# Kernel tuning notes

Hardware: AMD Instinct MI355X
Metric: run time of the kernel (lower is better)

The kernel has to match this reference:

```python
import jax, jax.numpy as jnp
import numpy as np

VOXEL_SIZE = np.array([0.05, 0.05, 0.1], dtype=np.float32)
PCR = np.array([0.0, -40.0, -3.0, 70.4, 40.0, 1.0], dtype=np.float32)
MAX_POINTS = 32
MAX_VOXELS = 120000
N_POINTS = 2_000_000
NFEAT = 4

GRID = np.round((PCR[3:] - PCR[:3]) / VOXEL_SIZE).astype(np.int64)  # [gx, gy, gz] = [1408, 1600, 40]
GX, GY, GZ = int(GRID[0]), int(GRID[1]), int(GRID[2])
G_TOTAL = GX * GY * GZ  # sentinel linear id for invalid points


def setup_inputs() -> dict:
    key = jax.random.key(0)
    k1, k2 = jax.random.split(key)
    # xyz uniform inside the point-cloud range, reflectivity ~ U[0,1)
    xyz = jax.random.uniform(k1, (N_POINTS, 3), minval=jnp.asarray(PCR[:3]), maxval=jnp.asarray(PCR[3:]))
    feat = jax.random.uniform(k2, (N_POINTS, NFEAT - 3))
    points = jnp.concatenate([xyz, feat], axis=1).astype(jnp.float32)
    return {"points": points}


def reference(points):
    """Deterministic hard voxelization (mmcv hard_voxelize_forward).

    Returns padded fixed-shape outputs plus voxel_num (jit-compatible):
      voxels [MAX_VOXELS, MAX_POINTS, C], coors [MAX_VOXELS, 3] (z,y,x),
      num_points_per_voxel [MAX_VOXELS], voxel_num scalar.
    Rows >= voxel_num are zero padding (torch version slices them off).
    """
    N, C = points.shape
    vs = jnp.asarray(VOXEL_SIZE)
    lo = jnp.asarray(PCR[:3])

    # Voxel coordinate of each point (x, y, z order)
    c = jnp.floor((points[:, :3] - lo) / vs).astype(jnp.int32)  # [N,3]
    valid = jnp.all((c >= 0) & (c < jnp.array([GX, GY, GZ], jnp.int32)), axis=1)

    # Linear voxel id; invalid points -> sentinel G_TOTAL (sorts last)
    lin = (c[:, 2].astype(jnp.int64) * (GY * GX)
           + c[:, 1].astype(jnp.int64) * GX
           + c[:, 0].astype(jnp.int64))
    lin = jnp.where(valid, lin, G_TOTAL)

    # Stable sort by voxel id: within a voxel, points keep original order
    order = jnp.argsort(lin, stable=True)          # [N] original indices
    slin = lin[order]
    pos = jnp.arange(N)
    is_new = jnp.concatenate([jnp.array([True]), slin[1:] != slin[:-1]])  # group starts
    start_pos = jax.lax.cummax(jnp.where(is_new, pos, 0))  # start position of each point's group
    rank_in_group = pos - start_pos                         # arrival order within voxel
    valid_s = slin < G_TOTAL

    # Voxel slots are assigned in order of first point appearance (deterministic CUDA kernel).
    # At each group start, the group's first original point index is order[pos].
    group_key = jnp.where(is_new & valid_s, order, N)       # non-starts/invalid rank last
    slot_at_pos = jnp.argsort(jnp.argsort(group_key))       # rank among groups by first appearance
    slot = slot_at_pos[start_pos]                            # [N] voxel slot per point

    voxel_num = jnp.minimum(jnp.sum((is_new & valid_s).astype(jnp.int32)), MAX_VOXELS)

    keep = valid_s & (rank_in_group < MAX_POINTS) & (slot < MAX_VOXELS)
    slot_w = jnp.where(keep, slot, MAX_VOXELS)   # dropped points -> extra pad row
    rank_w = jnp.where(keep, rank_in_group, 0)

    voxels = jnp.zeros((MAX_VOXELS + 1, MAX_POINTS, C), points.dtype)
    voxels = voxels.at[slot_w, rank_w].set(points[order])[:MAX_VOXELS]

    czyx = c[order][:, ::-1]  # store coords in (z, y, x) order like mmcv
    coor_keep = is_new & valid_s & (slot < MAX_VOXELS)
    cslot = jnp.where(coor_keep, slot, MAX_VOXELS)
    coors = jnp.zeros((MAX_VOXELS + 1, 3), jnp.int32).at[cslot].set(czyx)[:MAX_VOXELS]

    num_points_per_voxel = (jnp.zeros((MAX_VOXELS + 1,), jnp.int32)
                            .at[slot_w].add(keep.astype(jnp.int32))[:MAX_VOXELS])

    return voxels, coors, num_points_per_voxel, voxel_num
```

## Files before the change

### kernel.cpp

```cpp
#include <hip/hip_runtime.h>


#define GX 1408
#define GY 1600
#define GZ 40
#define MAXV 120000
#define MAXP 32

#define BINSHIFT 15
#define NB 2750
#define BCAP 1024
#define TSIZE 2048
#define TMASK (TSIZE - 1)
#define PB 4

#define ABLK 512
#define APT 16
#define EMIT_SPB 8

typedef unsigned long long u64;
typedef unsigned int u32;
#define EMPTY64 0xFFFFFFFFFFFFFFFFull

__device__ __forceinline__ u32 hashw(u32 lin) {
  return (lin * 2654435761u) >> 21 & TMASK;
}

__global__ __launch_bounds__(ABLK) void k_bin(const float4* __restrict__ pts,
                                              u64* __restrict__ pairs,
                                              u32* __restrict__ bincnt, int n) {
  __shared__ u32 hist[NB];
  __shared__ u32 cursor[NB];
  int tid = threadIdx.x;
  for (int b = tid; b < NB; b += ABLK) hist[b] = 0;
  __syncthreads();

  int base0 = blockIdx.x * (ABLK * APT) + tid;
  int lin[APT];
#pragma unroll
  for (int j = 0; j < APT; ++j) {
    int i = base0 + j * ABLK;
    lin[j] = -1;
    if (i < n) {
      float4 p = pts[i];
      int cx = (int)floorf((p.x - 0.0f)   / 0.05f);
      int cy = (int)floorf((p.y - -40.0f) / 0.05f);
      int cz = (int)floorf((p.z - -3.0f)  / 0.1f);
      if ((cx >= 0) && (cx < GX) && (cy >= 0) && (cy < GY) && (cz >= 0) && (cz < GZ)) {
        lin[j] = cz * (GX * GY) + cy * GX + cx;
        atomicAdd(&hist[(u32)lin[j] >> BINSHIFT], 1u);
      }
    }
  }
  __syncthreads();
  for (int b = tid; b < NB; b += ABLK) {
    u32 c = hist[b];
    cursor[b] = c ? atomicAdd(&bincnt[b], c) : 0u;
  }
  __syncthreads();
#pragma unroll
  for (int j = 0; j < APT; ++j) {
    if (lin[j] >= 0) {
      int i = base0 + j * ABLK;
      u32 b = (u32)lin[j] >> BINSHIFT;
      u32 pos = atomicAdd(&cursor[b], 1u);
      if (pos < BCAP) pairs[(size_t)b * BCAP + pos] = ((u64)(u32)lin[j] << 32) | (u32)i;
    }
  }
}

__global__ __launch_bounds__(256) void k_build(const u64* __restrict__ pairs,
                                               const u32* __restrict__ bincnt,
                                               u32* __restrict__ Lvals,
                                               unsigned char* __restrict__ isleader) {
  __shared__ u64 tab[TSIZE];
  int tid = threadIdx.x;
  int b = blockIdx.x;
  for (int s = tid; s < TSIZE; s += 256) tab[s] = EMPTY64;
  __syncthreads();

  u32 cnt = bincnt[b];
  if (cnt > BCAP) cnt = BCAP;
  size_t base = (size_t)b * BCAP;

  for (u32 c0 = 0; c0 < cnt; c0 += 256u * PB) {
    u64 pr[PB]; u32 hh[PB]; u64 old[PB];
#pragma unroll
    for (int k = 0; k < PB; ++k) {
      u32 idx = c0 + tid + (u32)k * 256u;
      pr[k] = (idx < cnt) ? pairs[base + idx] : EMPTY64;
    }
#pragma unroll
    for (int k = 0; k < PB; ++k) {
      if (pr[k] != EMPTY64) {
        hh[k] = hashw((u32)(pr[k] >> 32));
        old[k] = atomicCAS(&tab[hh[k]], EMPTY64, pr[k]);
      }
    }
#pragma unroll
    for (int k = 0; k < PB; ++k) {
      if (pr[k] != EMPTY64) {
        u32 lin = (u32)(pr[k] >> 32), i = (u32)pr[k];
        u32 s = hh[k];
        u64 o = old[k];
        while (o != EMPTY64) {
          if ((u32)(o >> 32) == lin) {
            while ((u32)o > i) {
              u64 want = (o & 0xFFFFFFFF00000000ull) | (u64)i;
              u64 prev = atomicCAS(&tab[s], o, want);
              if (prev == o) break;
              o = prev;
            }
            break;
          }
          s = (s + 1) & TMASK;
          o = atomicCAS(&tab[s], EMPTY64, pr[k]);
        }
      }
    }
  }
  __syncthreads();

  for (u32 c0 = 0; c0 < cnt; c0 += 256u * PB) {
    u64 pr[PB];
#pragma unroll
    for (int k = 0; k < PB; ++k) {
      u32 idx = c0 + tid + (u32)k * 256u;
      pr[k] = (idx < cnt) ? pairs[base + idx] : EMPTY64;
    }
#pragma unroll
    for (int k = 0; k < PB; ++k) {
      if (pr[k] != EMPTY64) {
        u32 idx = c0 + tid + (u32)k * 256u;
        u32 lin = (u32)(pr[k] >> 32), i = (u32)pr[k];
        u32 s = hashw(lin);
        u64 e = tab[s];
        while ((u32)(e >> 32) != lin) { s = (s + 1) & TMASK; e = tab[s]; }
        u32 L = (u32)e;
        Lvals[base + idx] = L;
        if (L == i) isleader[i] = 1;
      }
    }
  }
}

__global__ __launch_bounds__(256) void k_rankA(const unsigned char* __restrict__ isl,
                                               u32* __restrict__ flag,
                                               u32* __restrict__ bsum, int nwords) {
  __shared__ u32 red[256];
  int t = threadIdx.x;
  int w = blockIdx.x * 256 + t;
  u32 bits = 0;
  if (w < nwords) {
    const uint4* p = (const uint4*)(isl + (size_t)w * 32);
    uint4 a = p[0], b4 = p[1];
    u32 wd[8] = {a.x, a.y, a.z, a.w, b4.x, b4.y, b4.z, b4.w};
#pragma unroll
    for (int k = 0; k < 8; ++k) {
      u32 v = wd[k];
      bits |= (((v >> 0) & 1u) | ((v >> 8) & 1u) << 1 |
               ((v >> 16) & 1u) << 2 | ((v >> 24) & 1u) << 3) << (4 * k);
    }
    flag[w] = bits;
  }
  red[t] = __popc(bits);
  __syncthreads();
  for (int off = 128; off > 0; off >>= 1) {
    if (t < off) red[t] += red[t + off];
    __syncthreads();
  }
  if (t == 0) bsum[blockIdx.x] = red[0];
}

__global__ __launch_bounds__(256) void k_rankB(u32* __restrict__ bsum,
                                               float* __restrict__ voxnum_out,
                                               int* __restrict__ lmax, int nbk) {
  __shared__ u32 sm[256];
  int t = threadIdx.x;
  u32 v = (t < nbk) ? bsum[t] : 0;
  sm[t] = v;
  __syncthreads();
  for (int off = 1; off < 256; off <<= 1) {
    u32 x = sm[t];
    u32 add = (t >= off) ? sm[t - off] : 0;
    __syncthreads();
    sm[t] = x + add;
    __syncthreads();
  }
  if (t < nbk) bsum[t] = sm[t] - v;
  if (t == 255) {
    u32 total = sm[255];
    *voxnum_out = (float)(total < MAXV ? total : (u32)MAXV);
    if (total < MAXV) *lmax = 0x7FFFFFFF;
  }
}

__global__ __launch_bounds__(256) void k_rankC(const u32* __restrict__ flag,
                                               const u32* __restrict__ bsum,
                                               u32* __restrict__ wordpfx,
                                               int* __restrict__ lmax, int nwords) {
  __shared__ u32 sm[256];
  int t = threadIdx.x;
  int w = blockIdx.x * 256 + t;
  u32 bits = (w < nwords) ? flag[w] : 0u;
  u32 c = __popc(bits);
  sm[t] = c;
  __syncthreads();
  for (int off = 1; off < 256; off <<= 1) {
    u32 x = sm[t];
    u32 add = (t >= off) ? sm[t - off] : 0;
    __syncthreads();
    sm[t] = x + add;
    __syncthreads();
  }
  u32 p = bsum[blockIdx.x] + sm[t] - c;
  if (w < nwords) {
    wordpfx[w] = p;
    if (p < MAXV && p + c >= MAXV) {
      int kth = MAXV - 1 - (int)p;
      u32 ww = bits;
      while (kth > 0) { ww &= ww - 1; --kth; }
      *lmax = (w << 5) | (__ffs(ww) - 1);
    }
  }
}

__global__ __launch_bounds__(256) void k_keep(const u64* __restrict__ pairs,
                                              const u32* __restrict__ bincnt,
                                              const u32* __restrict__ Lvals,
                                              const u32* __restrict__ flag,
                                              const u32* __restrict__ wordpfx,
                                              const int* __restrict__ lmaxp,
                                              int* __restrict__ bcnt,
                                              int* __restrict__ bucket,
                                              float* __restrict__ out_coors) {
  int tid = threadIdx.x;
  int b = blockIdx.x;
  u32 Lmax = (u32)*lmaxp;
  u32 cnt = bincnt[b];
  if (cnt > BCAP) cnt = BCAP;
  size_t base = (size_t)b * BCAP;

  for (u32 j = tid; j < cnt; j += 256) {
    u32 L = Lvals[base + j];
    if (L > Lmax) continue;
    u64 pr = pairs[base + j];
    u32 lin = (u32)(pr >> 32), i = (u32)pr;
    u32 w = L >> 5;
    u32 r = wordpfx[w] + __popc(flag[w] & ((1u << (L & 31)) - 1u));
    int pos = atomicAdd(&bcnt[r], 1);
    if (pos < MAXP) bucket[r * MAXP + pos] = (int)i;
    if (i == L) {
      int li = (int)lin;
      int x = li % GX;
      int t2 = li / GX;
      int y = t2 % GY;
      int z = t2 / GY;
      out_coors[r * 3 + 0] = (float)z;
      out_coors[r * 3 + 1] = (float)y;
      out_coors[r * 3 + 2] = (float)x;
    }
  }
}

__global__ __launch_bounds__(256) void k_emit(const float4* __restrict__ pts,
                                              const int* __restrict__ bcnt,
                                              const int* __restrict__ bucket,
                                              float4* __restrict__ out_voxels,
                                              float* __restrict__ out_npts) {
  __shared__ int sb[EMIT_SPB][MAXP];
  int grp = threadIdx.x >> 5;
  int r = threadIdx.x & 31;
  int s = blockIdx.x * EMIT_SPB + grp;
  if (s >= MAXV) return;

  int nfull = bcnt[s];
  int m = nfull < MAXP ? nfull : MAXP;
  if (r < m) sb[grp][r] = bucket[s * MAXP + r];
  __syncthreads();

  float4 row = make_float4(0.f, 0.f, 0.f, 0.f);
  if (r < m) {
    int mine = -1;
    for (int jj = 0; jj < m; ++jj) {
      int ej = sb[grp][jj];
      int rk = 0;
      for (int kk2 = 0; kk2 < m; ++kk2) rk += (sb[grp][kk2] < ej) ? 1 : 0;
      if (rk == r) mine = ej;
    }
    row = pts[mine];
  }
  out_voxels[(size_t)s * MAXP + r] = row;
  if (r == 0) out_npts[s] = (float)m;
}

extern "C" void kernel_launch(void* const* d_in, const int* in_sizes, int n_in,
                              void* d_out, int out_size, void* d_ws, size_t ws_size,
                              hipStream_t stream) {
  const float4* pts = (const float4*)d_in[0];
  int n = in_sizes[0] / 4;
  float* out = (float*)d_out;
  int nwords = (n + 31) / 32;
  int nbk = (nwords + 255) / 256;

  char* ws = (char*)d_ws;
  size_t off = 0;
  u64* pairs    = (u64*)(ws + off); off += (size_t)NB * BCAP * 8;
  u32* Lvals    = (u32*)(ws + off); off += (size_t)NB * BCAP * 4;
  unsigned char* isleader = (unsigned char*)(ws + off); off += (size_t)n;
  u32* flag     = (u32*)(ws + off); off += 262144;
  u32* wordpfx  = (u32*)(ws + off); off += 262144;
  u32* bsum     = (u32*)(ws + off); off += 1024;
  u32* bincnt   = (u32*)(ws + off); off += 16384;
  int* lmax     = (int*)(ws + off); off += 64;
  int* bcnt     = (int*)(ws + off); off += (size_t)MAXV * 4;
  int* bucket   = (int*)(ws + off); off += (size_t)MAXV * MAXP * 4;

  float* out_voxels = out;
  float* out_coors  = out + (size_t)MAXV * MAXP * 4;
  float* out_npts   = out_coors + (size_t)MAXV * 3;

  hipMemsetAsync(bincnt, 0, 16384, stream);
  hipMemsetAsync(isleader, 0, (size_t)n, stream);
  hipMemsetAsync(bcnt, 0, (size_t)MAXV * 4, stream);
  hipMemsetAsync(out_coors, 0, ((size_t)MAXV * 3 + MAXV + 1) * sizeof(float), stream);

  int nb_bin = (n + ABLK * APT - 1) / (ABLK * APT);

  k_bin<<<nb_bin, ABLK, 0, stream>>>(pts, pairs, bincnt, n);
  k_build<<<NB, 256, 0, stream>>>(pairs, bincnt, Lvals, isleader);
  k_rankA<<<nbk, 256, 0, stream>>>(isleader, flag, bsum, nwords);
  k_rankB<<<1, 256, 0, stream>>>(bsum, out_npts + MAXV, lmax, nbk);
  k_rankC<<<nbk, 256, 0, stream>>>(flag, bsum, wordpfx, lmax, nwords);
  k_keep<<<NB, 256, 0, stream>>>(pairs, bincnt, Lvals, flag, wordpfx, lmax,
                                 bcnt, bucket, out_coors);
  k_emit<<<(MAXV + EMIT_SPB - 1) / EMIT_SPB, 256, 0, stream>>>(
      pts, bcnt, bucket, (float4*)out_voxels, out_npts);
}
```

Measured before the change: 175.8 us.

## Replace single-pass binning with two-level coarse/fine partition and fold rankB into rankC

```diff
diff --git a/kernel.cpp b/kernel.cpp
--- a/kernel.cpp
+++ b/kernel.cpp
@@ -7,15 +7,18 @@
 #define MAXV 120000
 #define MAXP 32
 
-#define BINSHIFT 15
-#define NB 2750
+#define CSHIFT 19
+#define NCB 172
+#define CCAP 14336
+#define FSHIFT 15
+#define NFB 2750
 #define BCAP 1024
 #define TSIZE 2048
 #define TMASK (TSIZE - 1)
 #define PB 4
 
 #define ABLK 512
-#define APT 16
+#define APT 8
 #define EMIT_SPB 8
 
 typedef unsigned long long u64;
@@ -26,13 +29,13 @@
   return (lin * 2654435761u) >> 21 & TMASK;
 }
 
-__global__ __launch_bounds__(ABLK) void k_bin(const float4* __restrict__ pts,
-                                              u64* __restrict__ pairs,
-                                              u32* __restrict__ bincnt, int n) {
-  __shared__ u32 hist[NB];
-  __shared__ u32 cursor[NB];
+__global__ __launch_bounds__(ABLK) void k_binA(const float4* __restrict__ pts,
+                                               u64* __restrict__ cpairs,
+                                               u32* __restrict__ ccnt, int n) {
+  __shared__ u32 hist[NCB];
+  __shared__ u32 cursor[NCB];
   int tid = threadIdx.x;
-  for (int b = tid; b < NB; b += ABLK) hist[b] = 0;
+  if (tid < NCB) hist[tid] = 0;
   __syncthreads();
 
   int base0 = blockIdx.x * (ABLK * APT) + tid;
@@ -48,29 +51,58 @@
       int cz = (int)floorf((p.z - -3.0f)  / 0.1f);
       if ((cx >= 0) && (cx < GX) && (cy >= 0) && (cy < GY) && (cz >= 0) && (cz < GZ)) {
         lin[j] = cz * (GX * GY) + cy * GX + cx;
-        atomicAdd(&hist[(u32)lin[j] >> BINSHIFT], 1u);
+        atomicAdd(&hist[(u32)lin[j] >> CSHIFT], 1u);
       }
     }
   }
   __syncthreads();
-  for (int b = tid; b < NB; b += ABLK) {
-    u32 c = hist[b];
-    cursor[b] = c ? atomicAdd(&bincnt[b], c) : 0u;
+  if (tid < NCB) {
+    u32 c = hist[tid];
+    cursor[tid] = c ? atomicAdd(&ccnt[tid], c) : 0u;
   }
   __syncthreads();
 #pragma unroll
   for (int j = 0; j < APT; ++j) {
     if (lin[j] >= 0) {
       int i = base0 + j * ABLK;
-      u32 b = (u32)lin[j] >> BINSHIFT;
-      u32 pos = atomicAdd(&cursor[b], 1u);
-      if (pos < BCAP) pairs[(size_t)b * BCAP + pos] = ((u64)(u32)lin[j] << 32) | (u32)i;
-    }
-  }
-}
-
-__global__ __launch_bounds__(256) void k_build(const u64* __restrict__ pairs,
-                                               const u32* __restrict__ bincnt,
+      u32 c = (u32)lin[j] >> CSHIFT;
+      u32 pos = atomicAdd(&cursor[c], 1u);
+      if (pos < CCAP) cpairs[(size_t)c * CCAP + pos] = ((u64)(u32)lin[j] << 32) | (u32)i;
+    }
+  }
+}
+
+__global__ __launch_bounds__(1024) void k_binB(const u64* __restrict__ cpairs,
+                                               const u32* __restrict__ ccnt,
+                                               u64* __restrict__ fpairs,
+                                               u32* __restrict__ fcnt) {
+  __shared__ u32 fh[16], fcur[16];
+  int tid = threadIdx.x;
+  int c = blockIdx.x;
+  if (tid < 16) { fh[tid] = 0; fcur[tid] = 0; }
+  __syncthreads();
+
+  u32 cnt = ccnt[c];
+  if (cnt > CCAP) cnt = CCAP;
+  size_t base = (size_t)c * CCAP;
+
+  for (u32 j = tid; j < cnt; j += 1024) {
+    u32 lin = (u32)(cpairs[base + j] >> 32);
+    atomicAdd(&fh[(lin >> FSHIFT) & 15], 1u);
+  }
+  __syncthreads();
+  if (tid < 16 && c * 16 + tid < NFB) fcnt[c * 16 + tid] = fh[tid];
+  __syncthreads();
+  for (u32 j = tid; j < cnt; j += 1024) {
+    u64 pr = cpairs[base + j];
+    u32 f = ((u32)(pr >> 32) >> FSHIFT) & 15;
+    u32 pos = atomicAdd(&fcur[f], 1u);
+    if (pos < BCAP) fpairs[(size_t)(c * 16 + f) * BCAP + pos] = pr;
+  }
+}
+
+__global__ __launch_bounds__(256) void k_build(const u64* __restrict__ fpairs,
+                                               const u32* __restrict__ fcnt,
                                                u32* __restrict__ Lvals,
                                                unsigned char* __restrict__ isleader) {
   __shared__ u64 tab[TSIZE];
@@ -79,67 +111,57 @@
   for (int s = tid; s < TSIZE; s += 256) tab[s] = EMPTY64;
   __syncthreads();
 
-  u32 cnt = bincnt[b];
+  u32 cnt = fcnt[b];
   if (cnt > BCAP) cnt = BCAP;
   size_t base = (size_t)b * BCAP;
 
-  for (u32 c0 = 0; c0 < cnt; c0 += 256u * PB) {
-    u64 pr[PB]; u32 hh[PB]; u64 old[PB];
-#pragma unroll
-    for (int k = 0; k < PB; ++k) {
-      u32 idx = c0 + tid + (u32)k * 256u;
-      pr[k] = (idx < cnt) ? pairs[base + idx] : EMPTY64;
-    }
-#pragma unroll
-    for (int k = 0; k < PB; ++k) {
-      if (pr[k] != EMPTY64) {
-        hh[k] = hashw((u32)(pr[k] >> 32));
-        old[k] = atomicCAS(&tab[hh[k]], EMPTY64, pr[k]);
+  u64 pr[PB]; u32 hh[PB]; u64 old[PB];
+#pragma unroll
+  for (int k = 0; k < PB; ++k) {
+    u32 idx = (u32)tid + (u32)k * 256u;
+    pr[k] = (idx < cnt) ? fpairs[base + idx] : EMPTY64;
+  }
+#pragma unroll
+  for (int k = 0; k < PB; ++k) {
+    if (pr[k] != EMPTY64) {
+      hh[k] = hashw((u32)(pr[k] >> 32));
+      old[k] = atomicCAS(&tab[hh[k]], EMPTY64, pr[k]);
+    }
+  }
+#pragma unroll
+  for (int k = 0; k < PB; ++k) {
+    if (pr[k] != EMPTY64) {
+      u32 lin = (u32)(pr[k] >> 32), i = (u32)pr[k];
+      u32 s = hh[k];
+      u64 o = old[k];
+      while (o != EMPTY64) {
+        if ((u32)(o >> 32) == lin) {
+          while ((u32)o > i) {
+            u64 want = (o & 0xFFFFFFFF00000000ull) | (u64)i;
+            u64 prev = atomicCAS(&tab[s], o, want);
+            if (prev == o) break;
+            o = prev;
+          }
+          break;
+        }
+        s = (s + 1) & TMASK;
+        o = atomicCAS(&tab[s], EMPTY64, pr[k]);
       }
     }
-#pragma unroll
-    for (int k = 0; k < PB; ++k) {
-      if (pr[k] != EMPTY64) {
-        u32 lin = (u32)(pr[k] >> 32), i = (u32)pr[k];
-        u32 s = hh[k];
-        u64 o = old[k];
-        while (o != EMPTY64) {
-          if ((u32)(o >> 32) == lin) {
-            while ((u32)o > i) {
-              u64 want = (o & 0xFFFFFFFF00000000ull) | (u64)i;
-              u64 prev = atomicCAS(&tab[s], o, want);
-              if (prev == o) break;
-              o = prev;
-            }
-            break;
-          }
-          s = (s + 1) & TMASK;
-          o = atomicCAS(&tab[s], EMPTY64, pr[k]);
-        }
-      }
-    }
-  }
-  __syncthreads();
-
-  for (u32 c0 = 0; c0 < cnt; c0 += 256u * PB) {
-    u64 pr[PB];
-#pragma unroll
-    for (int k = 0; k < PB; ++k) {
-      u32 idx = c0 + tid + (u32)k * 256u;
-      pr[k] = (idx < cnt) ? pairs[base + idx] : EMPTY64;
-    }
-#pragma unroll
-    for (int k = 0; k < PB; ++k) {
-      if (pr[k] != EMPTY64) {
-        u32 idx = c0 + tid + (u32)k * 256u;
-        u32 lin = (u32)(pr[k] >> 32), i = (u32)pr[k];
-        u32 s = hashw(lin);
-        u64 e = tab[s];
-        while ((u32)(e >> 32) != lin) { s = (s + 1) & TMASK; e = tab[s]; }
-        u32 L = (u32)e;
-        Lvals[base + idx] = L;
-        if (L == i) isleader[i] = 1;
-      }
+  }
+  __syncthreads();
+
+#pragma unroll
+  for (int k = 0; k < PB; ++k) {
+    if (pr[k] != EMPTY64) {
+      u32 idx = (u32)tid + (u32)k * 256u;
+      u32 lin = (u32)(pr[k] >> 32), i = (u32)pr[k];
+      u32 s = hashw(lin);
+      u64 e = tab[s];
+      while ((u32)(e >> 32) != lin) { s = (s + 1) & TMASK; e = tab[s]; }
+      u32 L = (u32)e;
+      Lvals[base + idx] = L;
+      if (L == i) isleader[i] = 1;
     }
   }
 }
@@ -172,35 +194,27 @@
   if (t == 0) bsum[blockIdx.x] = red[0];
 }
 
-__global__ __launch_bounds__(256) void k_rankB(u32* __restrict__ bsum,
-                                               float* __restrict__ voxnum_out,
-                                               int* __restrict__ lmax, int nbk) {
-  __shared__ u32 sm[256];
-  int t = threadIdx.x;
-  u32 v = (t < nbk) ? bsum[t] : 0;
-  sm[t] = v;
-  __syncthreads();
-  for (int off = 1; off < 256; off <<= 1) {
-    u32 x = sm[t];
-    u32 add = (t >= off) ? sm[t - off] : 0;
-    __syncthreads();
-    sm[t] = x + add;
-    __syncthreads();
-  }
-  if (t < nbk) bsum[t] = sm[t] - v;
-  if (t == 255) {
-    u32 total = sm[255];
-    *voxnum_out = (float)(total < MAXV ? total : (u32)MAXV);
-    if (total < MAXV) *lmax = 0x7FFFFFFF;
-  }
-}
-
 __global__ __launch_bounds__(256) void k_rankC(const u32* __restrict__ flag,
                                                const u32* __restrict__ bsum,
                                                u32* __restrict__ wordpfx,
-                                               int* __restrict__ lmax, int nwords) {
+                                               float* __restrict__ voxnum_out,
+                                               int* __restrict__ lmax,
+                                               int nwords, int nbk) {
+  __shared__ u32 sb_[256];
   __shared__ u32 sm[256];
   int t = threadIdx.x;
+  sb_[t] = (t < nbk) ? bsum[t] : 0;
+  __syncthreads();
+  for (int off = 1; off < 256; off <<= 1) {
+    u32 x = sb_[t];
+    u32 add = (t >= off) ? sb_[t - off] : 0;
+    __syncthreads();
+    sb_[t] = x + add;
+    __syncthreads();
+  }
+  u32 blockoff = (blockIdx.x > 0) ? sb_[blockIdx.x - 1] : 0u;
+  u32 total = sb_[nbk - 1];
+
   int w = blockIdx.x * 256 + t;
   u32 bits = (w < nwords) ? flag[w] : 0u;
   u32 c = __popc(bits);
@@ -213,7 +227,7 @@
     sm[t] = x + add;
     __syncthreads();
   }
-  u32 p = bsum[blockIdx.x] + sm[t] - c;
+  u32 p = blockoff + sm[t] - c;
   if (w < nwords) {
     wordpfx[w] = p;
     if (p < MAXV && p + c >= MAXV) {
@@ -223,10 +237,14 @@
       *lmax = (w << 5) | (__ffs(ww) - 1);
     }
   }
-}
-
-__global__ __launch_bounds__(256) void k_keep(const u64* __restrict__ pairs,
-                                              const u32* __restrict__ bincnt,
+  if (blockIdx.x == 0 && t == 0) {
+    *voxnum_out = (float)(total < MAXV ? total : (u32)MAXV);
+    if (total < MAXV) *lmax = 0x7FFFFFFF;
+  }
+}
+
+__global__ __launch_bounds__(256) void k_keep(const u64* __restrict__ fpairs,
+                                              const u32* __restrict__ fcnt,
                                               const u32* __restrict__ Lvals,
                                               const u32* __restrict__ flag,
                                               const u32* __restrict__ wordpfx,
@@ -237,14 +255,14 @@
   int tid = threadIdx.x;
   int b = blockIdx.x;
   u32 Lmax = (u32)*lmaxp;
-  u32 cnt = bincnt[b];
+  u32 cnt = fcnt[b];
   if (cnt > BCAP) cnt = BCAP;
   size_t base = (size_t)b * BCAP;
 
   for (u32 j = tid; j < cnt; j += 256) {
     u32 L = Lvals[base + j];
     if (L > Lmax) continue;
-    u64 pr = pairs[base + j];
+    u64 pr = fpairs[base + j];
     u32 lin = (u32)(pr >> 32), i = (u32)pr;
     u32 w = L >> 5;
     u32 r = wordpfx[w] + __popc(flag[w] & ((1u << (L & 31)) - 1u));
@@ -272,7 +290,6 @@
   int grp = threadIdx.x >> 5;
   int r = threadIdx.x & 31;
   int s = blockIdx.x * EMIT_SPB + grp;
-  if (s >= MAXV) return;
 
   int nfull = bcnt[s];
   int m = nfull < MAXP ? nfull : MAXP;
@@ -305,35 +322,37 @@
 
   char* ws = (char*)d_ws;
   size_t off = 0;
-  u64* pairs    = (u64*)(ws + off); off += (size_t)NB * BCAP * 8;
-  u32* Lvals    = (u32*)(ws + off); off += (size_t)NB * BCAP * 4;
-  unsigned char* isleader = (unsigned char*)(ws + off); off += (size_t)n;
-  u32* flag     = (u32*)(ws + off); off += 262144;
-  u32* wordpfx  = (u32*)(ws + off); off += 262144;
-  u32* bsum     = (u32*)(ws + off); off += 1024;
-  u32* bincnt   = (u32*)(ws + off); off += 16384;
-  int* lmax     = (int*)(ws + off); off += 64;
-  int* bcnt     = (int*)(ws + off); off += (size_t)MAXV * 4;
-  int* bucket   = (int*)(ws + off); off += (size_t)MAXV * MAXP * 4;
+  auto alloc = [&](size_t bytes) { void* p = ws + off; off += (bytes + 255) & ~(size_t)255; return p; };
+  u64* cpairs   = (u64*)alloc((size_t)NCB * CCAP * 8);
+  u64* fpairs   = (u64*)alloc((size_t)NFB * BCAP * 8);
+  u32* Lvals    = (u32*)alloc((size_t)NFB * BCAP * 4);
+  unsigned char* isleader = (unsigned char*)alloc((size_t)n);
+  u32* flag     = (u32*)alloc(262144);
+  u32* wordpfx  = (u32*)alloc(262144);
+  u32* bsum     = (u32*)alloc(1024);
+  int* lmax     = (int*)alloc(256);
+  u32* ccnt     = (u32*)alloc((size_t)NCB * 4 + (size_t)NFB * 4 + (size_t)MAXV * 4);
+  u32* fcnt     = ccnt + NCB;
+  int* bcnt     = (int*)(fcnt + NFB);
+  int* bucket   = (int*)alloc((size_t)MAXV * MAXP * 4);
 
   float* out_voxels = out;
   float* out_coors  = out + (size_t)MAXV * MAXP * 4;
   float* out_npts   = out_coors + (size_t)MAXV * 3;
 
-  hipMemsetAsync(bincnt, 0, 16384, stream);
+  hipMemsetAsync(ccnt, 0, ((size_t)NCB + NFB + MAXV) * 4, stream);
   hipMemsetAsync(isleader, 0, (size_t)n, stream);
-  hipMemsetAsync(bcnt, 0, (size_t)MAXV * 4, stream);
   hipMemsetAsync(out_coors, 0, ((size_t)MAXV * 3 + MAXV + 1) * sizeof(float), stream);
 
-  int nb_bin = (n + ABLK * APT - 1) / (ABLK * APT);
-
-  k_bin<<<nb_bin, ABLK, 0, stream>>>(pts, pairs, bincnt, n);
-  k_build<<<NB, 256, 0, stream>>>(pairs, bincnt, Lvals, isleader);
+  int nb_binA = (n + ABLK * APT - 1) / (ABLK * APT);
+
+  k_binA<<<nb_binA, ABLK, 0, stream>>>(pts, cpairs, ccnt, n);
+  k_binB<<<NCB, 1024, 0, stream>>>(cpairs, ccnt, fpairs, fcnt);
+  k_build<<<NFB, 256, 0, stream>>>(fpairs, fcnt, Lvals, isleader);
   k_rankA<<<nbk, 256, 0, stream>>>(isleader, flag, bsum, nwords);
-  k_rankB<<<1, 256, 0, stream>>>(bsum, out_npts + MAXV, lmax, nbk);
-  k_rankC<<<nbk, 256, 0, stream>>>(flag, bsum, wordpfx, lmax, nwords);
-  k_keep<<<NB, 256, 0, stream>>>(pairs, bincnt, Lvals, flag, wordpfx, lmax,
-                                 bcnt, bucket, out_coors);
-  k_emit<<<(MAXV + EMIT_SPB - 1) / EMIT_SPB, 256, 0, stream>>>(
+  k_rankC<<<nbk, 256, 0, stream>>>(flag, bsum, wordpfx, out_npts + MAXV, lmax, nwords, nbk);
+  k_keep<<<NFB, 256, 0, stream>>>(fpairs, fcnt, Lvals, flag, wordpfx, lmax,
+                                  bcnt, bucket, out_coors);
+  k_emit<<<MAXV / EMIT_SPB, 256, 0, stream>>>(
       pts, bcnt, bucket, (float4*)out_voxels, out_npts);
 }
```

Measured after the change: 177.2 us. No clear change (+0.8%).
